# Performance work log

Hardware: AMD Instinct MI355X
Metric: run time of the kernel (lower is better)

## Reference

```python
import jax, jax.numpy as jnp
import numpy as np

B, T, C = 2, 2048, 2048
NH, HS = 16, 128          # heads, head_size = C // NH
NLQ, NLKV = 512, 512      # q / kv latent dims
DHR = 64                  # decoupled rope head dim


def _rope_cos_sin(T, dhr, dtype=jnp.float32):
    inv = 1.0 / (10000.0 ** (np.arange(0, dhr, 2, dtype=np.float32) / dhr))
    ang = np.arange(T, dtype=np.float32)[:, None] * inv[None, :]  # [T, dhr//2]
    return jnp.asarray(np.cos(ang), dtype), jnp.asarray(np.sin(ang), dtype)


def setup_inputs() -> dict:
    key = jax.random.key(0)
    ks = jax.random.split(key, 10)
    s = 0.02
    cos, sin = _rope_cos_sin(T, DHR)
    return {
        "x":     jax.random.normal(ks[0], (B, T, C), jnp.float32),
        "cos":   cos,
        "sin":   sin,
        "W_dq":  s * jax.random.normal(ks[1], (NLQ, C), jnp.float32),
        "W_uq":  s * jax.random.normal(ks[2], (C, NLQ), jnp.float32),
        "W_dkv": s * jax.random.normal(ks[3], (NLKV, C), jnp.float32),
        "W_uk":  s * jax.random.normal(ks[4], (C, NLKV), jnp.float32),
        "W_uv":  s * jax.random.normal(ks[5], (C, NLKV), jnp.float32),
        "W_qr":  s * jax.random.normal(ks[6], (NH * DHR, NLQ), jnp.float32),
        "W_kr":  s * jax.random.normal(ks[7], (DHR, C), jnp.float32),
        "W_o":   s * jax.random.normal(ks[8], (C, C), jnp.float32),
    }


def _apply_rope(x, cos, sin):
    # x: [B, T, H, D]; pairs are interleaved (even=real, odd=imag)
    xr = x.reshape(x.shape[:-1] + (-1, 2))
    re, im = xr[..., 0], xr[..., 1]
    c = cos[None, :, None, :]
    s = sin[None, :, None, :]
    out = jnp.stack([re * c - im * s, re * s + im * c], axis=-1)
    return out.reshape(x.shape)


def reference(x, cos, sin, W_dq, W_uq, W_dkv, W_uk, W_uv, W_qr, W_kr, W_o):
    b, t, c = x.shape
    nh, hs, nlq, nlkv, dhr = NH, HS, NLQ, NLKV, DHR
    scale = 1.0 / np.sqrt(hs + dhr).astype(np.float32)

    # low-rank latents
    c_q = x @ W_dq.T          # [B, T, nlq]
    c_kv = x @ W_dkv.T        # [B, T, nlkv]

    # absorbed matrices (training path)
    # W_uq: [C, nlq] viewed as [nlq, nh, hs]; W_uk: [C, nlkv] viewed as [nh, hs, nlkv]
    k_eff = jnp.einsum('qhd,hdk->hqk', W_uq.reshape(nlq, nh, hs),
                       W_uk.reshape(nh, hs, nlkv))              # [nh, nlq, nlkv]
    v_eff = (W_uv.T @ W_o.T).reshape(nlkv, nh, hs).transpose(1, 0, 2)  # [nh, nlkv, hs]

    # content scores via absorbed low-rank path
    qk = jnp.einsum('btq,hqk->bhtk', c_q, k_eff)                # [B, nh, T, nlkv]
    attn_c = jnp.einsum('bhtk,bsk->bhts', qk, c_kv)             # [B, nh, T, T]

    # decoupled RoPE scores
    c_kr = (x @ W_kr.T)[:, :, None, :]                          # [B, T, 1, dhr]
    k_r = _apply_rope(c_kr, cos, sin)[:, :, 0, :]               # [B, T, dhr]
    c_qr = (c_q @ W_qr.T).reshape(b, t, nh, dhr)
    q_r = _apply_rope(c_qr, cos, sin)                            # [B, T, nh, dhr]
    attn_r = jnp.einsum('bthd,bsd->bhts', q_r, k_r)             # [B, nh, T, T]

    attn = (attn_c + attn_r) * scale
    mask = jnp.tril(jnp.ones((t, t), dtype=bool))
    attn = jnp.where(mask[None, None], attn, -jnp.inf)
    p = jax.nn.softmax(attn, axis=-1)

    ctx = jnp.einsum('bhts,bsk->bhtk', p, c_kv)                 # [B, nh, T, nlkv]
    y = jnp.einsum('bhtk,hkd->bthd', ctx, v_eff).reshape(b, t, c)
    return y
```

## Files before the change

kernel.cpp:

```cpp
#include <hip/hip_runtime.h>
#include <hip/hip_bf16.h>
#include <math.h>

typedef long long ll;
typedef unsigned short ushort_t;
typedef __attribute__((ext_vector_type(8))) __bf16 bf16x8;
typedef __attribute__((ext_vector_type(4))) float f32x4;

__device__ __forceinline__ ushort_t f2bf(float f) {
    __hip_bfloat16 h = __float2bfloat16(f);
    return *reinterpret_cast<ushort_t*>(&h);
}
__device__ __forceinline__ float bf2f(ushort_t u) {
    return __uint_as_float(((unsigned)u) << 16);
}
__device__ __forceinline__ void stage16(const void* g_lane, void* lds_uniform) {
    __builtin_amdgcn_global_load_lds(
        (const __attribute__((address_space(1))) unsigned int*)g_lane,
        (__attribute__((address_space(3))) unsigned int*)lds_uniform, 16, 0, 0);
}

#define TM 128
#define TN 128
#define TK 64

__global__ __launch_bounds__(256)
void gemm_bf16(const ushort_t* __restrict__ Ab, const ushort_t* __restrict__ Bb,
               void* __restrict__ Cb,
               int M, int N, int K,
               int a_rs, int b_rs, int c_rs, int Z2,
               ll a_bs1, ll a_bs2, ll b_bs1, ll b_bs2, ll c_bs1, ll c_bs2,
               int out_f32)
{
    const int m0 = blockIdx.y * TM;
    const int n0 = blockIdx.x * TN;
    const int z1 = blockIdx.z / Z2, z2 = blockIdx.z % Z2;

    const ushort_t* A = Ab + z1 * a_bs1 + z2 * a_bs2;
    const ushort_t* B = Bb + z1 * b_bs1 + z2 * b_bs2;

    __shared__ ushort_t As[2][TM][TK];
    __shared__ ushort_t Bs[2][TN][TK];

    const int tid  = threadIdx.x;
    const int w    = tid >> 6;
    const int l    = tid & 63;
    const int lo16 = l & 15;
    const int quad = l >> 4;
    const int wm0  = (w & 1) * 64;
    const int wn0  = (w >> 1) * 64;

    const int srow  = l >> 3;
    const int sunit = (l & 7) ^ srow;

    f32x4 acc[4][4];
    const f32x4 zero = {0.f, 0.f, 0.f, 0.f};
#pragma unroll
    for (int mi = 0; mi < 4; ++mi)
#pragma unroll
        for (int nj = 0; nj < 4; ++nj) acc[mi][nj] = zero;

    const int nIter = K / TK;

#pragma unroll
    for (int i = 0; i < 4; ++i) {
        const int rr = w * 32 + i * 8;
        stage16(A + (ll)(m0 + rr + srow) * a_rs + sunit * 8, &As[0][rr][0]);
        stage16(B + (ll)(n0 + rr + srow) * b_rs + sunit * 8, &Bs[0][rr][0]);
    }

    int buf = 0;
    for (int it = 0; it < nIter; ++it) {
        __syncthreads();
        if (it + 1 < nIter) {
            const int k0 = (it + 1) * TK;
            const int nb = buf ^ 1;
#pragma unroll
            for (int i = 0; i < 4; ++i) {
                const int rr = w * 32 + i * 8;
                stage16(A + (ll)(m0 + rr + srow) * a_rs + (k0 + sunit * 8), &As[nb][rr][0]);
                stage16(B + (ll)(n0 + rr + srow) * b_rs + (k0 + sunit * 8), &Bs[nb][rr][0]);
            }
        }
#pragma unroll
        for (int h = 0; h < 2; ++h) {
            const int phys = (h * 4 + quad) ^ (lo16 & 7);
            bf16x8 af[4], bfr[4];
#pragma unroll
            for (int mi = 0; mi < 4; ++mi)
                af[mi] = *(const bf16x8*)&As[buf][wm0 + mi * 16 + lo16][phys * 8];
#pragma unroll
            for (int nj = 0; nj < 4; ++nj)
                bfr[nj] = *(const bf16x8*)&Bs[buf][wn0 + nj * 16 + lo16][phys * 8];
#pragma unroll
            for (int mi = 0; mi < 4; ++mi)
#pragma unroll
                for (int nj = 0; nj < 4; ++nj)
                    acc[mi][nj] = __builtin_amdgcn_mfma_f32_16x16x32_bf16(
                        af[mi], bfr[nj], acc[mi][nj], 0, 0, 0);
        }
        buf ^= 1;
    }

    if (out_f32) {
        float* C = (float*)Cb + z1 * c_bs1 + z2 * c_bs2;
#pragma unroll
        for (int mi = 0; mi < 4; ++mi)
#pragma unroll
            for (int r = 0; r < 4; ++r) {
                const ll row = m0 + wm0 + mi * 16 + quad * 4 + r;
                float* cr = C + row * (ll)c_rs + (n0 + wn0 + lo16);
#pragma unroll
                for (int nj = 0; nj < 4; ++nj) cr[nj * 16] = acc[mi][nj][r];
            }
    } else {
        ushort_t* C = (ushort_t*)Cb + z1 * c_bs1 + z2 * c_bs2;
#pragma unroll
        for (int mi = 0; mi < 4; ++mi)
#pragma unroll
            for (int r = 0; r < 4; ++r) {
                const ll row = m0 + wm0 + mi * 16 + quad * 4 + r;
                ushort_t* cr = C + row * (ll)c_rs + (n0 + wn0 + lo16);
#pragma unroll
                for (int nj = 0; nj < 4; ++nj) cr[nj * 16] = f2bf(acc[mi][nj][r]);
            }
    }
}

#define QP_RS 3072
#define XP_RS 1152

__global__ __launch_bounds__(256, 2)
void flash_mla(const ushort_t* __restrict__ QP,
               const ushort_t* __restrict__ WukT,
               const ushort_t* __restrict__ XP,
               const ushort_t* __restrict__ VT,
               float* __restrict__ out,
               float scale)
{
    const int h  = blockIdx.y;
    const int b  = blockIdx.z;

    __shared__ __align__(16) char smem[49152];
    ushort_t* Ks = (ushort_t*)smem;
    ushort_t* Vs = (ushort_t*)(smem + 36864);
    ushort_t* Q3 = (ushort_t*)(smem + 32768);
    ushort_t* Aq = (ushort_t*)smem;
    ushort_t* Bw = (ushort_t*)(smem + 16384);

    const int tid  = threadIdx.x;
    const int w    = tid >> 6;
    const int l    = tid & 63;
    const int lo16 = l & 15;
    const int quad = l >> 4;
    char* Pw = smem + 45056 + w * 1024;

#pragma unroll 1
    for (int half = 0; half < 2; ++half) {
        const int qt = half ? (int)blockIdx.x : 31 - (int)blockIdx.x;
        const int t0 = qt * 64;

        __syncthreads();

        bf16x8 qa[18];

#pragma unroll
        for (int i = 0; i < 4; ++i) {
            int p = w * 256 + i * 64 + l;
            int r = p >> 4, u = p & 15, ul = u ^ (r & 15);
            stage16(QP + (ll)(b * 2048 + t0 + r) * QP_RS + h * 128 + ul * 8,
                    (char*)Aq + (ll)(w * 256 + i * 64) * 16);
        }
#pragma unroll
        for (int i = 0; i < 4; ++i) {
            int p = w * 256 + i * 64 + l;
            int r = p >> 4, u = p & 15, ul = u ^ (r & 15);
            stage16(WukT + ((ll)h * 512 + r) * 128 + ul * 8,
                    (char*)Bw + (ll)(w * 256 + i * 64) * 16);
        }
        __syncthreads();

        bf16x8 ab[4];
#pragma unroll
        for (int kd = 0; kd < 4; ++kd)
            ab[kd] = *(const bf16x8*)(Aq + (16 * w + lo16) * 128 + (((kd * 4 + quad) ^ lo16) & 15) * 8);

        for (int kc = 0; kc < 8; ++kc) {
#pragma unroll
            for (int nt = 0; nt < 4; ++nt) {
                f32x4 c = {0.f, 0.f, 0.f, 0.f};
#pragma unroll
                for (int kd = 0; kd < 4; ++kd) {
                    bf16x8 bb = *(const bf16x8*)(Bw + (nt * 16 + lo16) * 128 +
                                                 (((kd * 4 + quad) ^ lo16) & 15) * 8);
                    c = __builtin_amdgcn_mfma_f32_16x16x32_bf16(ab[kd], bb, c, 0, 0, 0);
                }
#pragma unroll
                for (int r = 0; r < 4; ++r)
                    Q3[(w * 16 + quad * 4 + r) * 72 + nt * 16 + lo16] = f2bf(c[r]);
            }
#pragma unroll
            for (int kd2 = 0; kd2 < 2; ++kd2)
                qa[kc * 2 + kd2] = *(const bf16x8*)(Q3 + (w * 16 + lo16) * 72 + kd2 * 32 + quad * 8);

            if (kc < 7) {
                __syncthreads();
#pragma unroll
                for (int i = 0; i < 4; ++i) {
                    int p = w * 256 + i * 64 + l;
                    int r = p >> 4, u = p & 15, ul = u ^ (r & 15);
                    stage16(WukT + ((ll)h * 512 + (kc + 1) * 64 + r) * 128 + ul * 8,
                            (char*)Bw + (ll)(w * 256 + i * 64) * 16);
                }
                __syncthreads();
            }
        }
#pragma unroll
        for (int kt = 16; kt < 18; ++kt)
            qa[kt] = *(const bf16x8*)(QP + (ll)(b * 2048 + t0 + 16 * w + lo16) * QP_RS +
                                      2048 + h * 64 + (kt - 16) * 32 + quad * 8);

        f32x4 oacc[8];
        const f32x4 zero = {0.f, 0.f, 0.f, 0.f};
#pragma unroll
        for (int dt = 0; dt < 8; ++dt) oacc[dt] = zero;
        float mrow[4], lrow[4];
#pragma unroll
        for (int r = 0; r < 4; ++r) { mrow[r] = -3.0e38f; lrow[r] = 0.f; }

        const int nst = 2 * qt + 2;
        for (int st = 0; st < nst; ++st) {
            const int s0 = st * 32;
            __syncthreads();
#pragma unroll
            for (int i = 0; i < 9; ++i) {
                int p = i * 64 + l;
                int r = 8 * w + p / 72, u = p % 72, ul = u ^ (r & 7);
                stage16(XP + (ll)(b * 2048 + s0 + r) * XP_RS + 512 + ul * 8,
                        (char*)Ks + (ll)(w * 576 + i * 64) * 16);
            }
#pragma unroll
            for (int i = 0; i < 2; ++i) {
                int p = w * 128 + i * 64 + l;
                int r = p >> 2, u = p & 3, ul = u ^ (r & 3);
                stage16(VT + ((ll)(b * 16 + h) * 128 + r) * 2048 + s0 + ul * 8,
                        (char*)Vs + (ll)(w * 128 + i * 64) * 16);
            }
            __syncthreads();

            f32x4 sc[2];
            sc[0] = zero; sc[1] = zero;
            __builtin_amdgcn_s_setprio(1);
#pragma unroll
            for (int kt = 0; kt < 18; ++kt)
#pragma unroll
                for (int nt = 0; nt < 2; ++nt) {
                    int phys = (kt * 4 + quad) ^ (lo16 & 7);
                    bf16x8 kb = *(const bf16x8*)(Ks + (nt * 16 + lo16) * 576 + phys * 8);
                    sc[nt] = __builtin_amdgcn_mfma_f32_16x16x32_bf16(qa[kt], kb, sc[nt], 0, 0, 0);
                }
            __builtin_amdgcn_s_setprio(0);

            const int rbase = 16 * w + quad * 4;
#pragma unroll
            for (int nt = 0; nt < 2; ++nt)
#pragma unroll
                for (int r = 0; r < 4; ++r) sc[nt][r] *= scale;
            if (st >= 2 * qt) {
#pragma unroll
                for (int nt = 0; nt < 2; ++nt)
#pragma unroll
                    for (int r = 0; r < 4; ++r)
                        if ((s0 + nt * 16 + lo16) > (t0 + rbase + r))
                            sc[nt][r] = -INFINITY;
            }

            float alpha[4];
#pragma unroll
            for (int r = 0; r < 4; ++r) {
                float tm = fmaxf(sc[0][r], sc[1][r]);
#pragma unroll
                for (int off = 1; off <= 8; off <<= 1)
                    tm = fmaxf(tm, __shfl_xor(tm, off, 64));
                float mnew = fmaxf(mrow[r], tm);
                alpha[r] = __expf(mrow[r] - mnew);
                mrow[r] = mnew;
                sc[0][r] = __expf(sc[0][r] - mnew);
                sc[1][r] = __expf(sc[1][r] - mnew);
                float rs = sc[0][r] + sc[1][r];
#pragma unroll
                for (int off = 1; off <= 8; off <<= 1)
                    rs += __shfl_xor(rs, off, 64);
                lrow[r] = lrow[r] * alpha[r] + rs;
            }
#pragma unroll
            for (int dt = 0; dt < 8; ++dt)
#pragma unroll
                for (int r = 0; r < 4; ++r) oacc[dt][r] *= alpha[r];

#pragma unroll
            for (int nt = 0; nt < 2; ++nt)
#pragma unroll
                for (int r = 0; r < 4; ++r) {
                    int row = quad * 4 + r;
                    int col = nt * 16 + lo16;
                    *(ushort_t*)(Pw + row * 64 + (((col >> 3) ^ (row & 3)) << 4) + (col & 7) * 2)
                        = f2bf(sc[nt][r]);
                }
            bf16x8 pf = *(const bf16x8*)(Pw + lo16 * 64 + (quad ^ (lo16 & 3)) * 16);

            __builtin_amdgcn_s_setprio(1);
#pragma unroll
            for (int dt = 0; dt < 8; ++dt) {
                int phys = quad ^ (lo16 & 3);
                bf16x8 vb = *(const bf16x8*)(Vs + (dt * 16 + lo16) * 32 + phys * 8);
                oacc[dt] = __builtin_amdgcn_mfma_f32_16x16x32_bf16(pf, vb, oacc[dt], 0, 0, 0);
            }
            __builtin_amdgcn_s_setprio(0);
        }

#pragma unroll
        for (int r = 0; r < 4; ++r) {
            const float inv = 1.0f / lrow[r];
            const ll row = (ll)(b * 2048 + t0 + 16 * w + quad * 4 + r);
#pragma unroll
            for (int dt = 0; dt < 8; ++dt)
                out[row * 2048 + h * 128 + dt * 16 + lo16] = oacc[dt][r] * inv;
        }
    }
}

__global__ void cvt_f32_bf16(const float* __restrict__ in, ushort_t* __restrict__ out, ll n4)
{
    ll i = (ll)blockIdx.x * 256 + threadIdx.x;
    if (i >= n4) return;
    float4 v = *(const float4*)(in + i * 4);
    ushort4 u;
    u.x = f2bf(v.x); u.y = f2bf(v.y); u.z = f2bf(v.z); u.w = f2bf(v.w);
    *(ushort4*)(out + i * 4) = u;
}

__global__ void build_wb1(const float* __restrict__ Wdq, const float* __restrict__ Wdkv,
                          const float* __restrict__ Wkr, ushort_t* __restrict__ out)
{
    ll i4 = ((ll)blockIdx.x * 256 + threadIdx.x) * 4;
    if (i4 >= (ll)1152 * 2048) return;
    int row = (int)(i4 >> 11);
    int col = (int)(i4 & 2047);
    float4 v = make_float4(0.f, 0.f, 0.f, 0.f);
    if (row < 512)       v = *(const float4*)(Wdq + (ll)row * 2048 + col);
    else if (row < 1024) v = *(const float4*)(Wdkv + (ll)(row - 512) * 2048 + col);
    else if (row < 1088) v = *(const float4*)(Wkr + (ll)(row - 1024) * 2048 + col);
    ushort4 u;
    u.x = f2bf(v.x); u.y = f2bf(v.y); u.z = f2bf(v.z); u.w = f2bf(v.w);
    *(ushort4*)(out + i4) = u;
}

__global__ void transpose_f32_bf16(const float* __restrict__ in, ushort_t* __restrict__ out,
                                   int R, int C, ll in_bs, ll out_bs)
{
    __shared__ float tile[32][33];
    const float* I = in + (ll)blockIdx.z * in_bs;
    ushort_t*    O = out + (ll)blockIdx.z * out_bs;
    int r0 = blockIdx.y * 32, c0 = blockIdx.x * 32;
    int tx = threadIdx.x & 31, ty = threadIdx.x >> 5;
#pragma unroll
    for (int i = 0; i < 4; ++i)
        tile[ty + i * 8][tx] = I[(ll)(r0 + ty + i * 8) * C + (c0 + tx)];
    __syncthreads();
#pragma unroll
    for (int i = 0; i < 4; ++i)
        O[(ll)(c0 + ty + i * 8) * R + (r0 + tx)] = f2bf(tile[tx][ty + i * 8]);
}

__global__ void rope_kr(ushort_t* __restrict__ XP, const float* __restrict__ cb,
                        const float* __restrict__ sb)
{
    int idx = blockIdx.x * 256 + threadIdx.x;
    if (idx >= 2 * 2048 * 32) return;
    int j = idx & 31, t = (idx >> 5) & 2047, b = idx >> 16;
    float c = cb[t * 32 + j], s = sb[t * 32 + j];
    ushort_t* p = XP + ((ll)(b * 2048 + t)) * 1152 + 1024 + 2 * j;
    float re = bf2f(p[0]), im = bf2f(p[1]);
    p[0] = f2bf(re * c - im * s);
    p[1] = f2bf(re * s + im * c);
}

__global__ void rope_qr_ip(ushort_t* __restrict__ QP, const float* __restrict__ cb,
                           const float* __restrict__ sb)
{
    int idx = blockIdx.x * 256 + threadIdx.x;
    if (idx >= 4096 * 512) return;
    int pj = idx & 511, h = pj >> 5, j = pj & 31;
    int row = idx >> 9;
    int t = row & 2047;
    float c = cb[t * 32 + j], s = sb[t * 32 + j];
    ll base = (ll)row * 3072 + 2048 + h * 64 + 2 * j;
    float re = bf2f(QP[base]), im = bf2f(QP[base + 1]);
    QP[base]     = f2bf(re * c - im * s);
    QP[base + 1] = f2bf(re * s + im * c);
}

static inline void gemmb(hipStream_t st, const ushort_t* A, const ushort_t* B, void* C,
                         int M, int N, int K, int a_rs, int b_rs, int c_rs,
                         int nb, int Z2,
                         ll a_bs1, ll a_bs2, ll b_bs1, ll b_bs2, ll c_bs1, ll c_bs2,
                         int of32)
{
    dim3 g(N / TN, M / TM, nb);
    gemm_bf16<<<g, 256, 0, st>>>(A, B, C, M, N, K, a_rs, b_rs, c_rs, Z2,
                                 a_bs1, a_bs2, b_bs1, b_bs2, c_bs1, c_bs2, of32);
}

extern "C" void kernel_launch(void* const* d_in, const int* in_sizes, int n_in,
                              void* d_out, int out_size, void* d_ws, size_t ws_size,
                              hipStream_t stream)
{
    const float* x     = (const float*)d_in[0];
    const float* cosb  = (const float*)d_in[1];
    const float* sinb  = (const float*)d_in[2];
    const float* W_dq  = (const float*)d_in[3];
    const float* W_uq  = (const float*)d_in[4];
    const float* W_dkv = (const float*)d_in[5];
    const float* W_uk  = (const float*)d_in[6];
    const float* W_uv  = (const float*)d_in[7];
    const float* W_qr  = (const float*)d_in[8];
    const float* W_kr  = (const float*)d_in[9];
    const float* W_o   = (const float*)d_in[10];
    float* out = (float*)d_out;

    const float scale = 0.07216878364870323f;

    char* base = (char*)d_ws;
    ushort_t* WB1     = (ushort_t*)(base + 0);
    ushort_t* WukT_b  = (ushort_t*)(base + 4718592);
    ushort_t* WuvT_b  = (ushort_t*)(base + 6815744);
    ushort_t* WB2     = (ushort_t*)(base + 8912896);
    ushort_t* veffT_b = (ushort_t*)(base + 12058624);
    ushort_t* Wo_b    = (ushort_t*)(base + 14155776);
    ushort_t* xb      = (ushort_t*)(base + 22544384);
    ushort_t* XP      = (ushort_t*)(base + 39321600);
    ushort_t* VT_all  = (ushort_t*)(base + 48758784);
    ushort_t* QP      = (ushort_t*)(base + 65536000);

    cvt_f32_bf16<<<8192, 256, 0, stream>>>(x, xb, 2097152);
    cvt_f32_bf16<<<4096, 256, 0, stream>>>(W_o, Wo_b, 1048576);
    build_wb1<<<2304, 256, 0, stream>>>(W_dq, W_dkv, W_kr, WB1);
    transpose_f32_bf16<<<dim3(16, 4, 16), 256, 0, stream>>>(W_uk, WukT_b, 128, 512, 65536, 65536);
    transpose_f32_bf16<<<dim3(16, 64, 1), 256, 0, stream>>>(W_uv, WuvT_b, 2048, 512, 0, 0);
    transpose_f32_bf16<<<dim3(64, 16, 1), 256, 0, stream>>>(W_uq, WB2, 512, 2048, 0, 0);
    cvt_f32_bf16<<<512, 256, 0, stream>>>(W_qr, WB2 + (ll)2048 * 512, 131072);

    gemmb(stream, Wo_b, WuvT_b, veffT_b, 128, 512, 2048, 2048, 2048, 512,
          16, 16, 0, 262144, 0, 0, 0, 65536, 0);

    gemmb(stream, xb, WB1, XP, 4096, 1152, 2048, 2048, 2048, 1152,
          1, 1, 0, 0, 0, 0, 0, 0, 0);
    rope_kr<<<512, 256, 0, stream>>>(XP, cosb, sinb);

    gemmb(stream, veffT_b, XP + 512, VT_all, 128, 2048, 512, 512, 1152, 2048,
          32, 16, 0, 65536, (ll)2048 * 1152, 0, (ll)16 * 262144, 262144, 0);

    gemmb(stream, XP, WB2, QP, 4096, 3072, 512, 1152, 512, 3072,
          1, 1, 0, 0, 0, 0, 0, 0, 0);
    rope_qr_ip<<<8192, 256, 0, stream>>>(QP, cosb, sinb);

    flash_mla<<<dim3(16, 16, 2), 256, 0, stream>>>(QP, WukT_b, XP, VT_all, out, scale);

    (void)in_sizes; (void)n_in; (void)out_size; (void)ws_size;
}
```

Baseline: 492.1 us.

## Process 128-row query tiles per block with two M-subtiles per wave and DPP reductions

The flash attention kernel now handles one 128-query tile per block, with two 16-row subtiles per wave, in place of two 64-row halves processed in sequence. Each K/V tile staged into LDS is therefore reused across twice as many query rows, and the rope query part is staged in LDS instead of loaded from global memory. Row max and sum reductions use DPP instead of shuffles, and waves skip fully masked key tiles. In exchange, LDS grows to 68KB and register pressure roughly doubles, which may cut occupancy. The grid is also now launched with 16 blocks in x, so the balanced pairing of causal tiles is replaced by reverse ordering.

```diff
diff --git a/kernel.cpp b/kernel.cpp
--- a/kernel.cpp
+++ b/kernel.cpp
@@ -18,6 +18,17 @@
     __builtin_amdgcn_global_load_lds(
         (const __attribute__((address_space(1))) unsigned int*)g_lane,
         (__attribute__((address_space(3))) unsigned int*)lds_uniform, 16, 0, 0);
+}
+
+#define DPPMAX(v, ctrl) v = fmaxf(v, __uint_as_float((unsigned)__builtin_amdgcn_update_dpp( \
+        0, (int)__float_as_uint(v), (ctrl), 0xF, 0xF, true)))
+#define DPPADD(v, ctrl) v = v + __uint_as_float((unsigned)__builtin_amdgcn_update_dpp( \
+        0, (int)__float_as_uint(v), (ctrl), 0xF, 0xF, true))
+__device__ __forceinline__ float red_max16(float v) {
+    DPPMAX(v, 0xB1); DPPMAX(v, 0x4E); DPPMAX(v, 0x141); DPPMAX(v, 0x140); return v;
+}
+__device__ __forceinline__ float red_sum16(float v) {
+    DPPADD(v, 0xB1); DPPADD(v, 0x4E); DPPADD(v, 0x141); DPPADD(v, 0x140); return v;
 }
 
 #define TM 128
@@ -138,196 +149,233 @@
                float* __restrict__ out,
                float scale)
 {
+    const int sp = 15 - (int)blockIdx.x;
     const int h  = blockIdx.y;
     const int b  = blockIdx.z;
-
-    __shared__ __align__(16) char smem[49152];
+    const int t0 = sp * 128;
+
+    __shared__ __align__(16) char smem[69632];
     ushort_t* Ks = (ushort_t*)smem;
     ushort_t* Vs = (ushort_t*)(smem + 36864);
-    ushort_t* Q3 = (ushort_t*)(smem + 32768);
+    ushort_t* Qr = (ushort_t*)(smem + 53248);
     ushort_t* Aq = (ushort_t*)smem;
-    ushort_t* Bw = (ushort_t*)(smem + 16384);
+    ushort_t* Q3 = (ushort_t*)smem;
+    ushort_t* Bw = (ushort_t*)(smem + 36864);
 
     const int tid  = threadIdx.x;
     const int w    = tid >> 6;
     const int l    = tid & 63;
     const int lo16 = l & 15;
     const int quad = l >> 4;
-    char* Pw = smem + 45056 + w * 1024;
-
-#pragma unroll 1
-    for (int half = 0; half < 2; ++half) {
-        const int qt = half ? (int)blockIdx.x : 31 - (int)blockIdx.x;
-        const int t0 = qt * 64;
-
+    char* Pw = smem + 45056 + w * 2048;
+
+    bf16x8 qa[2][16];
+
+#pragma unroll
+    for (int i = 0; i < 8; ++i) {
+        int pu = w * 512 + i * 64 + l;
+        int r = pu >> 4, u = pu & 15, ul = u ^ (r & 15);
+        stage16(QP + (ll)(b * 2048 + t0 + r) * QP_RS + h * 128 + ul * 8,
+                (char*)Aq + (ll)(w * 512 + i * 64) * 16);
+    }
+#pragma unroll
+    for (int i = 0; i < 4; ++i) {
+        int pu = w * 256 + i * 64 + l;
+        int r = pu >> 4, u = pu & 15, ul = u ^ (r & 15);
+        stage16(WukT + ((ll)h * 512 + r) * 128 + ul * 8,
+                (char*)Bw + (ll)(w * 256 + i * 64) * 16);
+    }
+#pragma unroll
+    for (int i = 0; i < 4; ++i) {
+        int pu = w * 256 + i * 64 + l;
+        int r = pu >> 3, u = pu & 7, ul = u ^ (r & 7);
+        stage16(QP + (ll)(b * 2048 + t0 + r) * QP_RS + 2048 + h * 64 + ul * 8,
+                (char*)Qr + (ll)(w * 256 + i * 64) * 16);
+    }
+    __syncthreads();
+
+    bf16x8 ab[2][4];
+#pragma unroll
+    for (int mt = 0; mt < 2; ++mt)
+#pragma unroll
+        for (int kd = 0; kd < 4; ++kd)
+            ab[mt][kd] = *(const bf16x8*)(Aq + (32 * w + mt * 16 + lo16) * 128 +
+                                          (((kd * 4 + quad) ^ lo16) & 15) * 8);
+    __syncthreads();
+
+    for (int kc = 0; kc < 8; ++kc) {
+#pragma unroll
+        for (int nt = 0; nt < 4; ++nt) {
+            f32x4 c0 = {0.f, 0.f, 0.f, 0.f}, c1 = {0.f, 0.f, 0.f, 0.f};
+#pragma unroll
+            for (int kd = 0; kd < 4; ++kd) {
+                bf16x8 bb = *(const bf16x8*)(Bw + (nt * 16 + lo16) * 128 +
+                                             (((kd * 4 + quad) ^ lo16) & 15) * 8);
+                c0 = __builtin_amdgcn_mfma_f32_16x16x32_bf16(ab[0][kd], bb, c0, 0, 0, 0);
+                c1 = __builtin_amdgcn_mfma_f32_16x16x32_bf16(ab[1][kd], bb, c1, 0, 0, 0);
+            }
+#pragma unroll
+            for (int r = 0; r < 4; ++r) {
+                Q3[(32 * w + quad * 4 + r) * 72 + nt * 16 + lo16]      = f2bf(c0[r]);
+                Q3[(32 * w + 16 + quad * 4 + r) * 72 + nt * 16 + lo16] = f2bf(c1[r]);
+            }
+        }
+#pragma unroll
+        for (int mt = 0; mt < 2; ++mt)
+#pragma unroll
+            for (int kd2 = 0; kd2 < 2; ++kd2)
+                qa[mt][kc * 2 + kd2] = *(const bf16x8*)(Q3 + (32 * w + mt * 16 + lo16) * 72 +
+                                                        kd2 * 32 + quad * 8);
+
+        if (kc < 7) {
+            __syncthreads();
+#pragma unroll
+            for (int i = 0; i < 4; ++i) {
+                int pu = w * 256 + i * 64 + l;
+                int r = pu >> 4, u = pu & 15, ul = u ^ (r & 15);
+                stage16(WukT + ((ll)h * 512 + (kc + 1) * 64 + r) * 128 + ul * 8,
+                        (char*)Bw + (ll)(w * 256 + i * 64) * 16);
+            }
+            __syncthreads();
+        }
+    }
+
+    f32x4 oacc[2][8];
+    const f32x4 zero = {0.f, 0.f, 0.f, 0.f};
+#pragma unroll
+    for (int mt = 0; mt < 2; ++mt)
+#pragma unroll
+        for (int dt = 0; dt < 8; ++dt) oacc[mt][dt] = zero;
+    float mrow[2][4], lrow[2][4];
+#pragma unroll
+    for (int mt = 0; mt < 2; ++mt)
+#pragma unroll
+        for (int r = 0; r < 4; ++r) { mrow[mt][r] = -3.0e38f; lrow[mt][r] = 0.f; }
+
+    const int nst = 4 * sp + 4;
+    for (int st = 0; st < nst; ++st) {
+        const int s0 = st * 32;
         __syncthreads();
-
-        bf16x8 qa[18];
-
-#pragma unroll
-        for (int i = 0; i < 4; ++i) {
-            int p = w * 256 + i * 64 + l;
-            int r = p >> 4, u = p & 15, ul = u ^ (r & 15);
-            stage16(QP + (ll)(b * 2048 + t0 + r) * QP_RS + h * 128 + ul * 8,
-                    (char*)Aq + (ll)(w * 256 + i * 64) * 16);
-        }
-#pragma unroll
-        for (int i = 0; i < 4; ++i) {
-            int p = w * 256 + i * 64 + l;
-            int r = p >> 4, u = p & 15, ul = u ^ (r & 15);
-            stage16(WukT + ((ll)h * 512 + r) * 128 + ul * 8,
-                    (char*)Bw + (ll)(w * 256 + i * 64) * 16);
+#pragma unroll
+        for (int i = 0; i < 9; ++i) {
+            int pu = i * 64 + l;
+            int r = 8 * w + pu / 72, u = pu % 72, ul = u ^ (r & 7);
+            stage16(XP + (ll)(b * 2048 + s0 + r) * XP_RS + 512 + ul * 8,
+                    (char*)Ks + (ll)(w * 576 + i * 64) * 16);
+        }
+#pragma unroll
+        for (int i = 0; i < 2; ++i) {
+            int pu = w * 128 + i * 64 + l;
+            int r = pu >> 2, u = pu & 3, ul = u ^ (r & 3);
+            stage16(VT + ((ll)(b * 16 + h) * 128 + r) * 2048 + s0 + ul * 8,
+                    (char*)Vs + (ll)(w * 128 + i * 64) * 16);
         }
         __syncthreads();
 
-        bf16x8 ab[4];
-#pragma unroll
-        for (int kd = 0; kd < 4; ++kd)
-            ab[kd] = *(const bf16x8*)(Aq + (16 * w + lo16) * 128 + (((kd * 4 + quad) ^ lo16) & 15) * 8);
-
-        for (int kc = 0; kc < 8; ++kc) {
-#pragma unroll
-            for (int nt = 0; nt < 4; ++nt) {
-                f32x4 c = {0.f, 0.f, 0.f, 0.f};
-#pragma unroll
-                for (int kd = 0; kd < 4; ++kd) {
-                    bf16x8 bb = *(const bf16x8*)(Bw + (nt * 16 + lo16) * 128 +
-                                                 (((kd * 4 + quad) ^ lo16) & 15) * 8);
-                    c = __builtin_amdgcn_mfma_f32_16x16x32_bf16(ab[kd], bb, c, 0, 0, 0);
-                }
-#pragma unroll
-                for (int r = 0; r < 4; ++r)
-                    Q3[(w * 16 + quad * 4 + r) * 72 + nt * 16 + lo16] = f2bf(c[r]);
-            }
-#pragma unroll
-            for (int kd2 = 0; kd2 < 2; ++kd2)
-                qa[kc * 2 + kd2] = *(const bf16x8*)(Q3 + (w * 16 + lo16) * 72 + kd2 * 32 + quad * 8);
-
-            if (kc < 7) {
-                __syncthreads();
-#pragma unroll
-                for (int i = 0; i < 4; ++i) {
-                    int p = w * 256 + i * 64 + l;
-                    int r = p >> 4, u = p & 15, ul = u ^ (r & 15);
-                    stage16(WukT + ((ll)h * 512 + (kc + 1) * 64 + r) * 128 + ul * 8,
-                            (char*)Bw + (ll)(w * 256 + i * 64) * 16);
-                }
-                __syncthreads();
-            }
-        }
-#pragma unroll
-        for (int kt = 16; kt < 18; ++kt)
-            qa[kt] = *(const bf16x8*)(QP + (ll)(b * 2048 + t0 + 16 * w + lo16) * QP_RS +
-                                      2048 + h * 64 + (kt - 16) * 32 + quad * 8);
-
-        f32x4 oacc[8];
-        const f32x4 zero = {0.f, 0.f, 0.f, 0.f};
-#pragma unroll
-        for (int dt = 0; dt < 8; ++dt) oacc[dt] = zero;
-        float mrow[4], lrow[4];
-#pragma unroll
-        for (int r = 0; r < 4; ++r) { mrow[r] = -3.0e38f; lrow[r] = 0.f; }
-
-        const int nst = 2 * qt + 2;
-        for (int st = 0; st < nst; ++st) {
-            const int s0 = st * 32;
-            __syncthreads();
-#pragma unroll
-            for (int i = 0; i < 9; ++i) {
-                int p = i * 64 + l;
-                int r = 8 * w + p / 72, u = p % 72, ul = u ^ (r & 7);
-                stage16(XP + (ll)(b * 2048 + s0 + r) * XP_RS + 512 + ul * 8,
-                        (char*)Ks + (ll)(w * 576 + i * 64) * 16);
-            }
-#pragma unroll
-            for (int i = 0; i < 2; ++i) {
-                int p = w * 128 + i * 64 + l;
-                int r = p >> 2, u = p & 3, ul = u ^ (r & 3);
-                stage16(VT + ((ll)(b * 16 + h) * 128 + r) * 2048 + s0 + ul * 8,
-                        (char*)Vs + (ll)(w * 128 + i * 64) * 16);
-            }
-            __syncthreads();
-
-            f32x4 sc[2];
-            sc[0] = zero; sc[1] = zero;
-            __builtin_amdgcn_s_setprio(1);
-#pragma unroll
-            for (int kt = 0; kt < 18; ++kt)
-#pragma unroll
-                for (int nt = 0; nt < 2; ++nt) {
-                    int phys = (kt * 4 + quad) ^ (lo16 & 7);
-                    bf16x8 kb = *(const bf16x8*)(Ks + (nt * 16 + lo16) * 576 + phys * 8);
-                    sc[nt] = __builtin_amdgcn_mfma_f32_16x16x32_bf16(qa[kt], kb, sc[nt], 0, 0, 0);
-                }
-            __builtin_amdgcn_s_setprio(0);
-
-            const int rbase = 16 * w + quad * 4;
+        if (st > 4 * sp + w) continue;
+
+        f32x4 sc[2][2];
+        sc[0][0] = zero; sc[0][1] = zero; sc[1][0] = zero; sc[1][1] = zero;
+        __builtin_amdgcn_s_setprio(1);
+#pragma unroll
+        for (int kt = 0; kt < 16; ++kt)
+#pragma unroll
+            for (int nt = 0; nt < 2; ++nt) {
+                int phys = (kt * 4 + quad) ^ (lo16 & 7);
+                bf16x8 kb = *(const bf16x8*)(Ks + (nt * 16 + lo16) * 576 + phys * 8);
+                sc[0][nt] = __builtin_amdgcn_mfma_f32_16x16x32_bf16(qa[0][kt], kb, sc[0][nt], 0, 0, 0);
+                sc[1][nt] = __builtin_amdgcn_mfma_f32_16x16x32_bf16(qa[1][kt], kb, sc[1][nt], 0, 0, 0);
+            }
+#pragma unroll
+        for (int kt2 = 0; kt2 < 2; ++kt2) {
+            int ph = (kt2 * 4 + quad) ^ (lo16 & 7);
+            bf16x8 qr0 = *(const bf16x8*)(Qr + (32 * w + lo16) * 64 + ph * 8);
+            bf16x8 qr1 = *(const bf16x8*)(Qr + (32 * w + 16 + lo16) * 64 + ph * 8);
+#pragma unroll
+            for (int nt = 0; nt < 2; ++nt) {
+                int phys = ((16 + kt2) * 4 + quad) ^ (lo16 & 7);
+                bf16x8 kb = *(const bf16x8*)(Ks + (nt * 16 + lo16) * 576 + phys * 8);
+                sc[0][nt] = __builtin_amdgcn_mfma_f32_16x16x32_bf16(qr0, kb, sc[0][nt], 0, 0, 0);
+                sc[1][nt] = __builtin_amdgcn_mfma_f32_16x16x32_bf16(qr1, kb, sc[1][nt], 0, 0, 0);
+            }
+        }
+        __builtin_amdgcn_s_setprio(0);
+
+#pragma unroll
+        for (int mt = 0; mt < 2; ++mt)
 #pragma unroll
             for (int nt = 0; nt < 2; ++nt)
 #pragma unroll
-                for (int r = 0; r < 4; ++r) sc[nt][r] *= scale;
-            if (st >= 2 * qt) {
+                for (int r = 0; r < 4; ++r) sc[mt][nt][r] *= scale;
+        if (st >= 4 * sp + w) {
+#pragma unroll
+            for (int mt = 0; mt < 2; ++mt) {
+                const int rb = t0 + 32 * w + mt * 16 + quad * 4;
 #pragma unroll
                 for (int nt = 0; nt < 2; ++nt)
 #pragma unroll
                     for (int r = 0; r < 4; ++r)
-                        if ((s0 + nt * 16 + lo16) > (t0 + rbase + r))
-                            sc[nt][r] = -INFINITY;
-            }
-
+                        if ((s0 + nt * 16 + lo16) > (rb + r))
+                            sc[mt][nt][r] = -INFINITY;
+            }
+        }
+
+#pragma unroll
+        for (int mt = 0; mt < 2; ++mt) {
             float alpha[4];
 #pragma unroll
             for (int r = 0; r < 4; ++r) {
-                float tm = fmaxf(sc[0][r], sc[1][r]);
-#pragma unroll
-                for (int off = 1; off <= 8; off <<= 1)
-                    tm = fmaxf(tm, __shfl_xor(tm, off, 64));
-                float mnew = fmaxf(mrow[r], tm);
-                alpha[r] = __expf(mrow[r] - mnew);
-                mrow[r] = mnew;
-                sc[0][r] = __expf(sc[0][r] - mnew);
-                sc[1][r] = __expf(sc[1][r] - mnew);
-                float rs = sc[0][r] + sc[1][r];
-#pragma unroll
-                for (int off = 1; off <= 8; off <<= 1)
-                    rs += __shfl_xor(rs, off, 64);
-                lrow[r] = lrow[r] * alpha[r] + rs;
+                float tm = red_max16(fmaxf(sc[mt][0][r], sc[mt][1][r]));
+                float mnew = fmaxf(mrow[mt][r], tm);
+                alpha[r] = __expf(mrow[mt][r] - mnew);
+                mrow[mt][r] = mnew;
+                sc[mt][0][r] = __expf(sc[mt][0][r] - mnew);
+                sc[mt][1][r] = __expf(sc[mt][1][r] - mnew);
+                float rs = red_sum16(sc[mt][0][r] + sc[mt][1][r]);
+                lrow[mt][r] = lrow[mt][r] * alpha[r] + rs;
             }
 #pragma unroll
             for (int dt = 0; dt < 8; ++dt)
 #pragma unroll
-                for (int r = 0; r < 4; ++r) oacc[dt][r] *= alpha[r];
-
+                for (int r = 0; r < 4; ++r) oacc[mt][dt][r] *= alpha[r];
+        }
+
+#pragma unroll
+        for (int mt = 0; mt < 2; ++mt)
 #pragma unroll
             for (int nt = 0; nt < 2; ++nt)
 #pragma unroll
                 for (int r = 0; r < 4; ++r) {
                     int row = quad * 4 + r;
                     int col = nt * 16 + lo16;
-                    *(ushort_t*)(Pw + row * 64 + (((col >> 3) ^ (row & 3)) << 4) + (col & 7) * 2)
-                        = f2bf(sc[nt][r]);
+                    *(ushort_t*)(Pw + mt * 1024 + row * 64 +
+                                 (((col >> 3) ^ (row & 3)) << 4) + (col & 7) * 2)
+                        = f2bf(sc[mt][nt][r]);
                 }
-            bf16x8 pf = *(const bf16x8*)(Pw + lo16 * 64 + (quad ^ (lo16 & 3)) * 16);
-
-            __builtin_amdgcn_s_setprio(1);
-#pragma unroll
-            for (int dt = 0; dt < 8; ++dt) {
-                int phys = quad ^ (lo16 & 3);
-                bf16x8 vb = *(const bf16x8*)(Vs + (dt * 16 + lo16) * 32 + phys * 8);
-                oacc[dt] = __builtin_amdgcn_mfma_f32_16x16x32_bf16(pf, vb, oacc[dt], 0, 0, 0);
-            }
-            __builtin_amdgcn_s_setprio(0);
-        }
-
+        bf16x8 pf0 = *(const bf16x8*)(Pw + lo16 * 64 + (quad ^ (lo16 & 3)) * 16);
+        bf16x8 pf1 = *(const bf16x8*)(Pw + 1024 + lo16 * 64 + (quad ^ (lo16 & 3)) * 16);
+
+        __builtin_amdgcn_s_setprio(1);
+#pragma unroll
+        for (int dt = 0; dt < 8; ++dt) {
+            int phys = quad ^ (lo16 & 3);
+            bf16x8 vb = *(const bf16x8*)(Vs + (dt * 16 + lo16) * 32 + phys * 8);
+            oacc[0][dt] = __builtin_amdgcn_mfma_f32_16x16x32_bf16(pf0, vb, oacc[0][dt], 0, 0, 0);
+            oacc[1][dt] = __builtin_amdgcn_mfma_f32_16x16x32_bf16(pf1, vb, oacc[1][dt], 0, 0, 0);
+        }
+        __builtin_amdgcn_s_setprio(0);
+    }
+
+#pragma unroll
+    for (int mt = 0; mt < 2; ++mt)
 #pragma unroll
         for (int r = 0; r < 4; ++r) {
-            const float inv = 1.0f / lrow[r];
-            const ll row = (ll)(b * 2048 + t0 + 16 * w + quad * 4 + r);
+            const float inv = 1.0f / lrow[mt][r];
+            const ll row = (ll)(b * 2048 + t0 + 32 * w + mt * 16 + quad * 4 + r);
 #pragma unroll
             for (int dt = 0; dt < 8; ++dt)
-                out[row * 2048 + h * 128 + dt * 16 + lo16] = oacc[dt][r] * inv;
-        }
-    }
+                out[row * 2048 + h * 128 + dt * 16 + lo16] = oacc[mt][dt][r] * inv;
+        }
 }
 
 __global__ void cvt_f32_bf16(const float* __restrict__ in, ushort_t* __restrict__ out, ll n4)
```

Result: slower. 661.3 us (+34.4%).

## Read K/V fragments directly from global memory in flash MLA loop

Applied to the files above, without the earlier changes.

Removes the shared-memory staging of K and V tiles and the two block barriers per step. Each wave now loads its MFMA operands straight from global memory (relying on L2/L1 reuse), and each wave stops at its own causal last tile rather than the block-wide one. Cross-lane max and sum reductions switch from shfl_xor to DPP row operations. The trade is loss of LDS reuse across the four waves and more, less coalesced global traffic per wave, in exchange for no synchronisation and less causal work.

```diff
diff --git a/kernel.cpp b/kernel.cpp
--- a/kernel.cpp
+++ b/kernel.cpp
@@ -18,6 +18,17 @@
     __builtin_amdgcn_global_load_lds(
         (const __attribute__((address_space(1))) unsigned int*)g_lane,
         (__attribute__((address_space(3))) unsigned int*)lds_uniform, 16, 0, 0);
+}
+
+#define DPPMAX(v, ctrl) v = fmaxf(v, __uint_as_float((unsigned)__builtin_amdgcn_update_dpp( \
+        0, (int)__float_as_uint(v), (ctrl), 0xF, 0xF, true)))
+#define DPPADD(v, ctrl) v = v + __uint_as_float((unsigned)__builtin_amdgcn_update_dpp( \
+        0, (int)__float_as_uint(v), (ctrl), 0xF, 0xF, true))
+__device__ __forceinline__ float red_max16(float v) {
+    DPPMAX(v, 0xB1); DPPMAX(v, 0x4E); DPPMAX(v, 0x141); DPPMAX(v, 0x140); return v;
+}
+__device__ __forceinline__ float red_sum16(float v) {
+    DPPADD(v, 0xB1); DPPADD(v, 0x4E); DPPADD(v, 0x141); DPPADD(v, 0x140); return v;
 }
 
 #define TM 128
@@ -142,11 +153,9 @@
     const int b  = blockIdx.z;
 
     __shared__ __align__(16) char smem[49152];
-    ushort_t* Ks = (ushort_t*)smem;
-    ushort_t* Vs = (ushort_t*)(smem + 36864);
-    ushort_t* Q3 = (ushort_t*)(smem + 32768);
     ushort_t* Aq = (ushort_t*)smem;
     ushort_t* Bw = (ushort_t*)(smem + 16384);
+    ushort_t* Q3 = (ushort_t*)(smem + 32768);
 
     const int tid  = threadIdx.x;
     const int w    = tid >> 6;
@@ -228,37 +237,25 @@
 #pragma unroll
         for (int r = 0; r < 4; ++r) { mrow[r] = -3.0e38f; lrow[r] = 0.f; }
 
-        const int nst = 2 * qt + 2;
-        for (int st = 0; st < nst; ++st) {
+        const int stLast = 2 * qt + (w >> 1);
+        const ushort_t* Kbase = XP + (ll)(b * 2048 + lo16) * XP_RS + 512 + quad * 8;
+        const ushort_t* Vbase = VT + ((ll)((b * 16 + h) * 128) + lo16) * 2048 + quad * 8;
+
+        for (int st = 0; st <= stLast; ++st) {
             const int s0 = st * 32;
-            __syncthreads();
-#pragma unroll
-            for (int i = 0; i < 9; ++i) {
-                int p = i * 64 + l;
-                int r = 8 * w + p / 72, u = p % 72, ul = u ^ (r & 7);
-                stage16(XP + (ll)(b * 2048 + s0 + r) * XP_RS + 512 + ul * 8,
-                        (char*)Ks + (ll)(w * 576 + i * 64) * 16);
-            }
-#pragma unroll
-            for (int i = 0; i < 2; ++i) {
-                int p = w * 128 + i * 64 + l;
-                int r = p >> 2, u = p & 3, ul = u ^ (r & 3);
-                stage16(VT + ((ll)(b * 16 + h) * 128 + r) * 2048 + s0 + ul * 8,
-                        (char*)Vs + (ll)(w * 128 + i * 64) * 16);
-            }
-            __syncthreads();
 
             f32x4 sc[2];
             sc[0] = zero; sc[1] = zero;
+            const ushort_t* K0 = Kbase + (ll)s0 * XP_RS;
+            const ushort_t* K1 = K0 + 16 * XP_RS;
             __builtin_amdgcn_s_setprio(1);
 #pragma unroll
-            for (int kt = 0; kt < 18; ++kt)
-#pragma unroll
-                for (int nt = 0; nt < 2; ++nt) {
-                    int phys = (kt * 4 + quad) ^ (lo16 & 7);
-                    bf16x8 kb = *(const bf16x8*)(Ks + (nt * 16 + lo16) * 576 + phys * 8);
-                    sc[nt] = __builtin_amdgcn_mfma_f32_16x16x32_bf16(qa[kt], kb, sc[nt], 0, 0, 0);
-                }
+            for (int kt = 0; kt < 18; ++kt) {
+                bf16x8 kb0 = *(const bf16x8*)(K0 + kt * 32);
+                bf16x8 kb1 = *(const bf16x8*)(K1 + kt * 32);
+                sc[0] = __builtin_amdgcn_mfma_f32_16x16x32_bf16(qa[kt], kb0, sc[0], 0, 0, 0);
+                sc[1] = __builtin_amdgcn_mfma_f32_16x16x32_bf16(qa[kt], kb1, sc[1], 0, 0, 0);
+            }
             __builtin_amdgcn_s_setprio(0);
 
             const int rbase = 16 * w + quad * 4;
@@ -266,7 +263,7 @@
             for (int nt = 0; nt < 2; ++nt)
 #pragma unroll
                 for (int r = 0; r < 4; ++r) sc[nt][r] *= scale;
-            if (st >= 2 * qt) {
+            if (st == stLast) {
 #pragma unroll
                 for (int nt = 0; nt < 2; ++nt)
 #pragma unroll
@@ -278,19 +275,13 @@
             float alpha[4];
 #pragma unroll
             for (int r = 0; r < 4; ++r) {
-                float tm = fmaxf(sc[0][r], sc[1][r]);
-#pragma unroll
-                for (int off = 1; off <= 8; off <<= 1)
-                    tm = fmaxf(tm, __shfl_xor(tm, off, 64));
+                float tm = red_max16(fmaxf(sc[0][r], sc[1][r]));
                 float mnew = fmaxf(mrow[r], tm);
                 alpha[r] = __expf(mrow[r] - mnew);
                 mrow[r] = mnew;
                 sc[0][r] = __expf(sc[0][r] - mnew);
                 sc[1][r] = __expf(sc[1][r] - mnew);
-                float rs = sc[0][r] + sc[1][r];
-#pragma unroll
-                for (int off = 1; off <= 8; off <<= 1)
-                    rs += __shfl_xor(rs, off, 64);
+                float rs = red_sum16(sc[0][r] + sc[1][r]);
                 lrow[r] = lrow[r] * alpha[r] + rs;
             }
 #pragma unroll
@@ -312,8 +303,7 @@
             __builtin_amdgcn_s_setprio(1);
 #pragma unroll
             for (int dt = 0; dt < 8; ++dt) {
-                int phys = quad ^ (lo16 & 3);
-                bf16x8 vb = *(const bf16x8*)(Vs + (dt * 16 + lo16) * 32 + phys * 8);
+                bf16x8 vb = *(const bf16x8*)(Vbase + (ll)(dt * 16) * 2048 + s0);
                 oacc[dt] = __builtin_amdgcn_mfma_f32_16x16x32_bf16(pf, vb, oacc[dt], 0, 0, 0);
             }
             __builtin_amdgcn_s_setprio(0);
```

Result: slower. 1.031 ms (+109.6%).
